# Kernel optimization log

Measured on AMD Instinct MI355X. Metric: run time of the kernel, lower is better.

## Reference

```python
import jax, jax.numpy as jnp
import numpy as np

B, N, C = 8, 1374, 768
H = 12
HD = C // H  # 64
HIDDEN = int(C * 4.0)  # 3072
EPS = 1e-5


def setup_inputs() -> dict:
    key = jax.random.key(0)
    ks = jax.random.split(key, 12)
    s = 0.02
    return {
        "x": jax.random.normal(ks[0], (B, N, C), jnp.float32),
        "rope_freqs": jax.random.normal(ks[1], (1, N, 1, HD), jnp.float32),
        "ln1_g": jnp.ones((C,), jnp.float32),
        "ln1_b": jnp.zeros((C,), jnp.float32),
        "qkv_w": jax.random.normal(ks[2], (3 * C, C), jnp.float32) * s,
        "qkv_b": jnp.zeros((3 * C,), jnp.float32),
        "proj_w": jax.random.normal(ks[3], (C, C), jnp.float32) * s,
        "proj_b": jnp.zeros((C,), jnp.float32),
        "ln2_g": jnp.ones((C,), jnp.float32),
        "ln2_b": jnp.zeros((C,), jnp.float32),
        "w1": jax.random.normal(ks[4], (HIDDEN, C), jnp.float32) * s,
        "b1": jnp.zeros((HIDDEN,), jnp.float32),
        "w2": jax.random.normal(ks[5], (HIDDEN, C), jnp.float32) * s,
        "b2": jnp.zeros((HIDDEN,), jnp.float32),
        "w3": jax.random.normal(ks[6], (C, HIDDEN), jnp.float32) * s,
        "b3": jnp.zeros((C,), jnp.float32),
    }


def _layernorm(x, g, b):
    mu = jnp.mean(x, axis=-1, keepdims=True)
    var = jnp.mean(jnp.square(x - mu), axis=-1, keepdims=True)
    return (x - mu) * jax.lax.rsqrt(var + EPS) * g + b


def _rotate_half(x):
    x1, x2 = jnp.split(x, 2, axis=-1)
    return jnp.concatenate([-x2, x1], axis=-1)


def _apply_rope(q, k, freqs):
    # freqs: [1, N, 1, HD] -> [1, 1, N, HD] (matches torch permute(0,2,1,3))
    f = jnp.transpose(freqs, (0, 2, 1, 3))
    cos, sin = jnp.cos(f), jnp.sin(f)
    q_rot = q * cos + _rotate_half(q) * sin
    k_rot = k * cos + _rotate_half(k) * sin
    return q_rot, k_rot


def reference(x, rope_freqs, ln1_g, ln1_b, qkv_w, qkv_b, proj_w, proj_b,
              ln2_g, ln2_b, w1, b1, w2, b2, w3, b3):
    scale = HD ** -0.5
    # --- Attention branch ---
    h = _layernorm(x, ln1_g, ln1_b)
    qkv = jnp.einsum('bnc,dc->bnd', h, qkv_w) + qkv_b          # [B,N,3C]
    qkv = qkv.reshape(B, N, 3, H, HD).transpose(2, 0, 3, 1, 4)  # [3,B,H,N,HD]
    q, k, v = qkv[0], qkv[1], qkv[2]
    # rope_freqs covers all N tokens -> n_special = 0 path
    q, k = _apply_rope(q, k, rope_freqs)
    attn = jnp.einsum('bhnd,bhmd->bhnm', q, k) * scale          # [B,H,N,N]
    attn = jax.nn.softmax(attn, axis=-1)
    o = jnp.einsum('bhnm,bhmd->bhnd', attn, v)                  # [B,H,N,HD]
    o = o.transpose(0, 2, 1, 3).reshape(B, N, C)
    o = jnp.einsum('bnc,dc->bnd', o, proj_w) + proj_b
    x = x + o
    # --- SwiGLU MLP branch ---
    h2 = _layernorm(x, ln2_g, ln2_b)
    x1 = jnp.einsum('bnc,hc->bnh', h2, w1) + b1
    x2 = jnp.einsum('bnc,hc->bnh', h2, w2) + b2
    hid = jax.nn.silu(x1) * x2
    mlp_out = jnp.einsum('bnh,ch->bnc', hid, w3) + b3
    return x + mlp_out
```

## Files before the change

### kernel.cpp

```cpp
#include <hip/hip_runtime.h>
#include <stdint.h>

#define B_ 8
#define N_ 1374
#define C_ 768
#define H_ 12
#define HD_ 64
#define HID_ 3072
#define M_ (B_*N_)
#define MPAD_ 11008
#define QT_ 22
#define QT2_ 11

#define QSC_ 0.18033688011112042f

typedef __attribute__((ext_vector_type(8))) short short8;
typedef __attribute__((ext_vector_type(4))) float f32x4;
typedef __attribute__((ext_vector_type(16))) float f32x16;
typedef __attribute__((ext_vector_type(4))) _Float16 half4;
typedef __attribute__((ext_vector_type(2))) _Float16 half2v;

__device__ __forceinline__ unsigned short f2bf(float f) {
  unsigned u = __float_as_uint(f);
  u += 0x7FFF + ((u >> 16) & 1);
  return (unsigned short)(u >> 16);
}
__device__ __forceinline__ float bf2f(unsigned short h) {
  return __uint_as_float(((unsigned)h) << 16);
}
__device__ __forceinline__ unsigned short f2h(float f) {
  return __builtin_bit_cast(unsigned short, (_Float16)f);
}

__device__ __forceinline__ half2v pkrtz(float a, float b) {
  return __builtin_bit_cast(half2v, __builtin_amdgcn_cvt_pkrtz(a, b));
}

#if __has_builtin(__builtin_amdgcn_global_load_lds)
#define HAVE_GLL 1
#endif

__device__ __forceinline__ void gld16(const unsigned short* g, unsigned short* l) {
#ifdef HAVE_GLL
  __builtin_amdgcn_global_load_lds((const __attribute__((address_space(1))) void*)g,
                                   (__attribute__((address_space(3))) void*)l, 16, 0, 0);
#else
  *(short8*)l = *(const short8*)g;
#endif
}

__device__ __forceinline__ void ln_body(const float* __restrict__ in,
    const float* __restrict__ g, const float* __restrict__ bta,
    unsigned short* __restrict__ out, int row, int t) {
  const float* xr = in + (size_t)row * C_;
  float v0 = xr[t], v1 = xr[t + 256], v2 = xr[t + 512];
  float s1 = v0 + v1 + v2;
  float s2 = v0*v0 + v1*v1 + v2*v2;
  for (int off = 1; off < 64; off <<= 1) {
    s1 += __shfl_xor(s1, off, 64);
    s2 += __shfl_xor(s2, off, 64);
  }
  __shared__ float r1[4], r2[4];
  int wave = t >> 6, lane = t & 63;
  if (lane == 0) { r1[wave] = s1; r2[wave] = s2; }
  __syncthreads();
  float tot1 = r1[0] + r1[1] + r1[2] + r1[3];
  float tot2 = r2[0] + r2[1] + r2[2] + r2[3];
  float mu = tot1 * (1.0f / C_);
  float var = tot2 * (1.0f / C_) - mu * mu;
  float rs = rsqrtf(var + 1e-5f);
  size_t ob = (size_t)row * C_;
  out[ob + t]       = f2bf((v0 - mu) * rs * g[t]       + bta[t]);
  out[ob + t + 256] = f2bf((v1 - mu) * rs * g[t + 256] + bta[t + 256]);
  out[ob + t + 512] = f2bf((v2 - mu) * rs * g[t + 512] + bta[t + 512]);
}

__global__ __launch_bounds__(256) void ln_kernel(const float* __restrict__ in,
    const float* __restrict__ g, const float* __restrict__ bta,
    unsigned short* __restrict__ out) {
  ln_body(in, g, bta, out, blockIdx.x, threadIdx.x);
}

__global__ __launch_bounds__(256) void cvt5_ln_kernel(
    const float* __restrict__ s0, const float* __restrict__ s1,
    const float* __restrict__ s2, const float* __restrict__ s3,
    const float* __restrict__ s4, unsigned short* __restrict__ out,
    const float* __restrict__ x, const float* __restrict__ ln_g,
    const float* __restrict__ ln_b, unsigned short* __restrict__ h) {
  int blk = blockIdx.x;
  if (blk < 9216) {
    int id = blk * 256 + threadIdx.x;
    const float* src; int off;
    if (id < 442368)        { src = s0; off = id; }
    else if (id < 589824)   { src = s1; off = id - 442368; }
    else if (id < 1179648)  { src = s2; off = id - 589824; }
    else if (id < 1769472)  { src = s3; off = id - 1179648; }
    else                    { src = s4; off = id - 1769472; }
    float4 v = ((const float4*)src)[off];
    ushort4 o;
    o.x = f2bf(v.x); o.y = f2bf(v.y); o.z = f2bf(v.z); o.w = f2bf(v.w);
    ((ushort4*)out)[id] = o;
  } else {
    ln_body(x, ln_g, ln_b, h, blk - 9216, threadIdx.x);
  }
}

template<int EPI, int ROPE, int TM, int SWZ>
__global__ __launch_bounds__(256, (TM == 64) ? 4 : 2) void gemm_bt(
    const unsigned short* __restrict__ A,
    const unsigned short* __restrict__ W,
    void* __restrict__ outp,
    const float* __restrict__ bias0,
    const float* __restrict__ resid,
    const float* __restrict__ freqs,
    int K, int ldo, int Mvalid, int X)
{
  constexpr int MI = TM / 32;
  __shared__ __align__(16) unsigned short As[2][TM * 32];
  __shared__ __align__(16) unsigned short Bs[2][4096];
  const int t = threadIdx.x;
  const int lane = t & 63;
  const int wave = t >> 6;
  const int wm = (wave >> 1) * (TM / 2);
  const int wn = (wave & 1) * 64;
  const int lr = lane & 15;
  const int lg = lane >> 4;
  const int lk = lg * 8;
  int bx, by;
  if (SWZ) {
    int Y = gridDim.x / X;
    int lin = blockIdx.x;
    int sgsz = X * 8;
    int sg = lin / sgsz;
    int base_y = sg * 8;
    int rows = Y - base_y; if (rows > 8) rows = 8;
    int within = lin - sg * sgsz;
    by = base_y + within % rows;
    bx = within / rows;
  } else {
    bx = blockIdx.x % X;
    by = blockIdx.x / X;
  }
  const int tm0 = by * TM;
  const int tn0 = bx * 128;
  const int r0 = t >> 2;
  const int c0 = (t & 3) * 8;
  const unsigned short* ga0 = A + (size_t)(tm0 + r0) * K + c0;
  const unsigned short* ga1 = A + (size_t)(tm0 + 64 + r0) * K + c0;
  const unsigned short* gb0 = W + (size_t)(tn0 + r0) * K + c0;
  const unsigned short* gb1 = W + (size_t)(tn0 + 64 + r0) * K + c0;
  f32x4 zero = {0.f, 0.f, 0.f, 0.f};
  f32x4 acc[MI][4];
#pragma unroll
  for (int mi = 0; mi < MI; ++mi)
#pragma unroll
    for (int ni = 0; ni < 4; ++ni) acc[mi][ni] = zero;

  for (int kt = 0; kt < K; kt += 64) {
    __syncthreads();
    gld16(ga0 + kt,      &As[0][t * 8]);
    gld16(ga0 + kt + 32, &As[1][t * 8]);
    if (TM == 128) {
      gld16(ga1 + kt,      &As[0][2048 + t * 8]);
      gld16(ga1 + kt + 32, &As[1][2048 + t * 8]);
    }
    gld16(gb0 + kt,      &Bs[0][t * 8]);
    gld16(gb1 + kt,      &Bs[0][2048 + t * 8]);
    gld16(gb0 + kt + 32, &Bs[1][t * 8]);
    gld16(gb1 + kt + 32, &Bs[1][2048 + t * 8]);
    __syncthreads();
#pragma unroll
    for (int u = 0; u < 2; ++u) {
      short8 af[MI], bfr[4];
#pragma unroll
      for (int mi = 0; mi < MI; ++mi) af[mi] = *(const short8*)&As[u][(wm + mi * 16 + lr) * 32 + lk];
#pragma unroll
      for (int ni = 0; ni < 4; ++ni) bfr[ni] = *(const short8*)&Bs[u][(wn + ni * 16 + lr) * 32 + lk];
#pragma unroll
      for (int mi = 0; mi < MI; ++mi)
#pragma unroll
        for (int ni = 0; ni < 4; ++ni)
          acc[mi][ni] = __builtin_amdgcn_mfma_f32_16x16x32_bf16(af[mi], bfr[ni], acc[mi][ni], 0, 0, 0);
    }
  }

  if (EPI == 0) {
    bool dorope = ROPE && ((tn0 + wn) < 1536);
    bool isq    = ROPE && ((tn0 + wn) < 768);
    bool isv    = ROPE && ((tn0 + wn) >= 1536);
#pragma unroll
    for (int mi = 0; mi < MI; ++mi) {
#pragma unroll
      for (int p = 0; p < 2; ++p) {
        int col1 = tn0 + wn + p * 16 + lr;
        int col2 = col1 + 32;
        float bv1 = bias0[col1], bv2 = bias0[col2];
        int e = p * 16 + lr;
#pragma unroll
        for (int r = 0; r < 4; ++r) {
          int row = tm0 + wm + mi * 16 + lg * 4 + r;
          float v1 = acc[mi][p][r] + bv1;
          float v2 = acc[mi][p + 2][r] + bv2;
          float o1 = v1, o2 = v2;
          if (dorope) {
            int n = row % N_;
            float f1 = freqs[n * HD_ + e];
            float f2 = freqs[n * HD_ + e + 32];
            float c1, s1, c2, s2;
            __sincosf(f1, &s1, &c1);
            __sincosf(f2, &s2, &c2);
            o1 = v1 * c1 - v2 * s1;
            o2 = v2 * c2 + v1 * s2;
          }
          if (isq) { o1 *= QSC_; o2 *= QSC_; }
          size_t base = (size_t)row * ldo;
          if (isv) {
            ((unsigned short*)outp)[base + col1] = f2h(o1);
            ((unsigned short*)outp)[base + col2] = f2h(o2);
          } else {
            ((unsigned short*)outp)[base + col1] = f2bf(o1);
            ((unsigned short*)outp)[base + col2] = f2bf(o2);
          }
        }
      }
    }
  } else {
#pragma unroll
    for (int mi = 0; mi < MI; ++mi) {
#pragma unroll
      for (int ni = 0; ni < 4; ++ni) {
        int col = tn0 + wn + ni * 16 + lr;
        float bval = bias0[col];
#pragma unroll
        for (int r = 0; r < 4; ++r) {
          int row = tm0 + wm + mi * 16 + lg * 4 + r;
          float v = acc[mi][ni][r] + bval;
          size_t idx = (size_t)row * ldo + col;
          if (EPI == 1) {
            if (row < Mvalid) ((float*)outp)[idx] = resid[idx] + v;
          } else {
            if (row < Mvalid) ((float*)outp)[idx] = ((float*)outp)[idx] + v;
          }
        }
      }
    }
  }
}

__global__ __launch_bounds__(256, 2) void gemm_w12_swiglu(
    const unsigned short* __restrict__ A,
    const unsigned short* __restrict__ W1,
    const unsigned short* __restrict__ W2,
    unsigned short* __restrict__ hid,
    const float* __restrict__ b1,
    const float* __restrict__ b2)
{
  __shared__ __align__(16) unsigned short As[2][4096];
  __shared__ __align__(16) unsigned short B1s[2][2048];
  __shared__ __align__(16) unsigned short B2s[2][2048];
  const int t = threadIdx.x;
  const int lane = t & 63;
  const int wave = t >> 6;
  const int wm = (wave >> 1) * 64;
  const int wn = (wave & 1) * 32;
  const int lr = lane & 15;
  const int lg = lane >> 4;
  const int lk = lg * 8;
  const int tm0 = blockIdx.y * 128;
  const int tn0 = blockIdx.x * 64;
  const int r0 = t >> 2;
  const int c0 = (t & 3) * 8;
  const unsigned short* ga0 = A + (size_t)(tm0 + r0) * 768 + c0;
  const unsigned short* ga1 = A + (size_t)(tm0 + 64 + r0) * 768 + c0;
  const unsigned short* g1 = W1 + (size_t)(tn0 + r0) * 768 + c0;
  const unsigned short* g2 = W2 + (size_t)(tn0 + r0) * 768 + c0;
  f32x4 zero = {0.f, 0.f, 0.f, 0.f};
  f32x4 acc1[4][2], acc2[4][2];
#pragma unroll
  for (int mi = 0; mi < 4; ++mi)
#pragma unroll
    for (int ni = 0; ni < 2; ++ni) { acc1[mi][ni] = zero; acc2[mi][ni] = zero; }

  for (int kt = 0; kt < 768; kt += 64) {
    __syncthreads();
    gld16(ga0 + kt,      &As[0][t * 8]);
    gld16(ga1 + kt,      &As[0][2048 + t * 8]);
    gld16(ga0 + kt + 32, &As[1][t * 8]);
    gld16(ga1 + kt + 32, &As[1][2048 + t * 8]);
    gld16(g1 + kt,       &B1s[0][t * 8]);
    gld16(g1 + kt + 32,  &B1s[1][t * 8]);
    gld16(g2 + kt,       &B2s[0][t * 8]);
    gld16(g2 + kt + 32,  &B2s[1][t * 8]);
    __syncthreads();
#pragma unroll
    for (int u = 0; u < 2; ++u) {
      short8 af[4], b1f[2], b2f[2];
#pragma unroll
      for (int mi = 0; mi < 4; ++mi) af[mi] = *(const short8*)&As[u][(wm + mi * 16 + lr) * 32 + lk];
#pragma unroll
      for (int ni = 0; ni < 2; ++ni) {
        b1f[ni] = *(const short8*)&B1s[u][(wn + ni * 16 + lr) * 32 + lk];
        b2f[ni] = *(const short8*)&B2s[u][(wn + ni * 16 + lr) * 32 + lk];
      }
#pragma unroll
      for (int mi = 0; mi < 4; ++mi)
#pragma unroll
        for (int ni = 0; ni < 2; ++ni) {
          acc1[mi][ni] = __builtin_amdgcn_mfma_f32_16x16x32_bf16(af[mi], b1f[ni], acc1[mi][ni], 0, 0, 0);
          acc2[mi][ni] = __builtin_amdgcn_mfma_f32_16x16x32_bf16(af[mi], b2f[ni], acc2[mi][ni], 0, 0, 0);
        }
    }
  }
#pragma unroll
  for (int mi = 0; mi < 4; ++mi) {
#pragma unroll
    for (int ni = 0; ni < 2; ++ni) {
      int col = tn0 + wn + ni * 16 + lr;
      float bv1 = b1[col], bv2 = b2[col];
#pragma unroll
      for (int r = 0; r < 4; ++r) {
        int row = tm0 + wm + mi * 16 + lg * 4 + r;
        float a1 = acc1[mi][ni][r] + bv1;
        float a2 = acc2[mi][ni][r] + bv2;
        float h = a1 / (1.f + __expf(-a1)) * a2;
        hid[(size_t)row * HID_ + col] = f2bf(h);
      }
    }
  }
}

struct FalseT { static constexpr bool value = false; };
struct TrueT  { static constexpr bool value = true;  };

__global__ __launch_bounds__(256, 3) void attn_kernel(
    const unsigned short* __restrict__ qkv,
    unsigned short* __restrict__ o2)
{
  __shared__ __align__(16) unsigned short Ks[2][64 * 88];
  __shared__ __align__(16) _Float16 Vt[2][64 * 72];
  int bidx = blockIdx.x;
  int qt = bidx % QT2_;
  int bh = bidx / QT2_;
  int head = bh % H_;
  int b = bh / H_;
  int t = threadIdx.x, lane = t & 63, wave = t >> 6;
  int lq = lane & 31, lg2 = lane >> 5;

  short8 bq[4];
  {
    int m = qt * 128 + wave * 32 + lq;
    int mc = (m < N_) ? m : (N_ - 1);
    const unsigned short* qrow = qkv + (size_t)(b * N_ + mc) * 2304 + head * HD_;
#pragma unroll
    for (int c = 0; c < 4; ++c)
      bq[c] = *(const short8*)(qrow + c * 16 + lg2 * 8);
  }

  f32x16 acc[2];
  f32x16 dacc;
  acc[0] = {}; acc[1] = {}; dacc = {};

  const int kr0 = t >> 3;
  const int kc  = (t & 7) * 8;
  const int vp  = t & 31;
  const int vc  = t >> 5;
  const unsigned short* kbase = qkv + (size_t)(b * N_) * 2304 + 768  + head * HD_ + kc;
  const unsigned short* vbase = qkv + (size_t)(b * N_) * 2304 + 1536 + head * HD_ + vc * 8;

  short8 krg[2], vrg[2];
  auto issue = [&](int jt) {
    int j0 = jt * 64 + kr0;        if (j0 >= N_) j0 = N_ - 1;
    int j1 = jt * 64 + kr0 + 32;   if (j1 >= N_) j1 = N_ - 1;
    int vj0 = jt * 64 + 2 * vp;    if (vj0 >= N_) vj0 = N_ - 1;
    int vj1 = jt * 64 + 2 * vp + 1; if (vj1 >= N_) vj1 = N_ - 1;
    krg[0] = *(const short8*)(kbase + (size_t)j0 * 2304);
    krg[1] = *(const short8*)(kbase + (size_t)j1 * 2304);
    vrg[0] = *(const short8*)(vbase + (size_t)vj0 * 2304);
    vrg[1] = *(const short8*)(vbase + (size_t)vj1 * 2304);
  };

  const half4 vones = {(_Float16)1.f, (_Float16)1.f, (_Float16)1.f, (_Float16)1.f};

  auto compute = [&](int jt, const unsigned short* ksb, const _Float16* vtb, auto tailc) {
    constexpr bool TAIL = decltype(tailc)::value;
#pragma unroll
    for (int st2 = 0; st2 < 2; ++st2) {
      f32x16 sc = {};
      {
        const unsigned short* krow = &ksb[(st2 * 32 + lq) * 88 + lg2 * 8];
        short8 ak0 = *(const short8*)(krow);
        short8 ak1 = *(const short8*)(krow + 16);
        short8 ak2 = *(const short8*)(krow + 32);
        short8 ak3 = *(const short8*)(krow + 48);
        sc = __builtin_amdgcn_mfma_f32_32x32x16_bf16(ak0, bq[0], sc, 0, 0, 0);
        sc = __builtin_amdgcn_mfma_f32_32x32x16_bf16(ak1, bq[1], sc, 0, 0, 0);
        sc = __builtin_amdgcn_mfma_f32_32x32x16_bf16(ak2, bq[2], sc, 0, 0, 0);
        sc = __builtin_amdgcn_mfma_f32_32x32x16_bf16(ak3, bq[3], sc, 0, 0, 0);
      }
#pragma unroll
      for (int r = 0; r < 16; ++r) {
        float pv = exp2f(sc[r]);
        if (TAIL) {
          int jw = (r & 3) + 8 * (r >> 2) + 4 * lg2;
          int j = jt * 64 + st2 * 32 + jw;
          pv = (j < N_) ? pv : 0.f;
        }
        sc[r] = pv;
      }
      half4 pf[4];
#pragma unroll
      for (int ks = 0; ks < 4; ++ks) {
        union { half4 v; half2v h[2]; } pu;
        pu.h[0] = pkrtz(sc[ks * 4 + 0], sc[ks * 4 + 1]);
        pu.h[1] = pkrtz(sc[ks * 4 + 2], sc[ks * 4 + 3]);
        pf[ks] = pu.v;
      }
#pragma unroll
      for (int ks = 0; ks < 4; ++ks)
        dacc = __builtin_amdgcn_mfma_f32_32x32x8f16(pf[ks], vones, dacc, 0, 0, 0);
#pragma unroll
      for (int dt = 0; dt < 2; ++dt) {
#pragma unroll
        for (int ks = 0; ks < 4; ++ks) {
          half4 bv = *(const half4*)&vtb[(dt * 32 + lq) * 72 + st2 * 32 + ks * 8 + lg2 * 4];
          acc[dt] = __builtin_amdgcn_mfma_f32_32x32x8f16(pf[ks], bv, acc[dt], 0, 0, 0);
        }
      }
    }
  };

  issue(0);
  int cur = 0;
  for (int jt = 0; jt < QT_; ++jt) {
    unsigned short* ksb = &Ks[cur][0];
    _Float16* vtb = &Vt[cur][0];
    *(short8*)&ksb[kr0 * 88 + kc] = krg[0];
    *(short8*)&ksb[(kr0 + 32) * 88 + kc] = krg[1];
#pragma unroll
    for (int i = 0; i < 8; ++i) {
      unsigned lo = (unsigned short)vrg[0][i];
      unsigned hi = (unsigned short)vrg[1][i];
      *(unsigned*)&Vt[cur][(vc * 8 + i) * 72 + 2 * vp] = lo | (hi << 16);
    }
    __syncthreads();
    issue(jt + 1);
    if (jt == QT_ - 1) compute(jt, ksb, vtb, TrueT{});
    else               compute(jt, ksb, vtb, FalseT{});
    cur ^= 1;
  }

#pragma unroll
  for (int r = 0; r < 16; ++r) {
    int qw = (r & 3) + 8 * (r >> 2) + 4 * lg2;
    int m = qt * 128 + wave * 32 + qw;
    if (m < N_) {
      float invd = 1.f / dacc[r];
      unsigned short* orow = o2 + (size_t)(b * N_ + m) * C_ + head * HD_ + lq;
      orow[0]  = f2bf(acc[0][r] * invd);
      orow[32] = f2bf(acc[1][r] * invd);
    }
  }
}

extern "C" void kernel_launch(void* const* d_in, const int* in_sizes, int n_in,
                              void* d_out, int out_size, void* d_ws, size_t ws_size,
                              hipStream_t stream) {
  const float* x      = (const float*)d_in[0];
  const float* freqs  = (const float*)d_in[1];
  const float* ln1_g  = (const float*)d_in[2];
  const float* ln1_b  = (const float*)d_in[3];
  const float* qkv_w  = (const float*)d_in[4];
  const float* qkv_b  = (const float*)d_in[5];
  const float* proj_w = (const float*)d_in[6];
  const float* proj_b = (const float*)d_in[7];
  const float* ln2_g  = (const float*)d_in[8];
  const float* ln2_b  = (const float*)d_in[9];
  const float* w1     = (const float*)d_in[10];
  const float* b1     = (const float*)d_in[11];
  const float* w2     = (const float*)d_in[12];
  const float* b2     = (const float*)d_in[13];
  const float* w3     = (const float*)d_in[14];
  const float* b3     = (const float*)d_in[15];
  float* out = (float*)d_out;
  char* ws = (char*)d_ws;

  unsigned short* hB     = (unsigned short*)(ws + 0);
  unsigned short* wqkvB  = (unsigned short*)(ws + 16908288);
  unsigned short* wprojB = (unsigned short*)(ws + 20447232);
  unsigned short* w12B   = (unsigned short*)(ws + 21626880);
  unsigned short* w3B    = (unsigned short*)(ws + 31064064);
  unsigned short* qkvB   = (unsigned short*)(ws + 35782656);
  unsigned short* o2B    = (unsigned short*)(ws + 86507520);
  unsigned short* hidB   = qkvB;

  cvt5_ln_kernel<<<9216 + M_, 256, 0, stream>>>(qkv_w, proj_w, w1, w2, w3, wqkvB,
                                                x, ln1_g, ln1_b, hB);

  gemm_bt<0, 1, 128, 1><<<18 * 86, 256, 0, stream>>>(hB, wqkvB, qkvB, qkv_b, nullptr, freqs, 768, 2304, M_, 18);
  attn_kernel<<<B_ * H_ * QT2_, 256, 0, stream>>>(qkvB, o2B);
  gemm_bt<1, 0, 64, 1><<<6 * 172, 256, 0, stream>>>(o2B, wprojB, out, proj_b, x, nullptr, 768, 768, M_, 6);

  ln_kernel<<<M_, 256, 0, stream>>>(out, ln2_g, ln2_b, hB);
  gemm_w12_swiglu<<<dim3(48, 86), 256, 0, stream>>>(hB, w12B, w12B + 3072 * 768, hidB, b1, b2);
  gemm_bt<3, 0, 128, 1><<<6 * 86, 256, 0, stream>>>(hidB, w3B, out, b3, nullptr, nullptr, 3072, 768, M_, 6);
}
```

Measured before the change: 526.7 us.

## Interleave W1/W2 rows and use 256x256 eight-wave pipelined SwiGLU GEMM

Weight conversion now interleaves W1 and W2 in 128-row blocks, so one 256-column tile of the combined weight covers matching halves of both projections. The SwiGLU GEMM is replaced by a 512-thread kernel with 256x256 tiles, a double-buffered 128KB LDS pipeline, explicit vmcnt waits, barriers and setprio around the MFMA blocks. The W2 half of the accumulators is exchanged through LDS for the epilogue. The aim is higher arithmetic intensity and latency hiding, at the cost of one block per CU from LDS use, fewer blocks overall, and fragile hand-scheduled synchronisation.

```diff
diff --git a/kernel.cpp b/kernel.cpp
--- a/kernel.cpp
+++ b/kernel.cpp
@@ -90,16 +90,26 @@
   int blk = blockIdx.x;
   if (blk < 9216) {
     int id = blk * 256 + threadIdx.x;
-    const float* src; int off;
+    const float* src; int off; int dest = id;
     if (id < 442368)        { src = s0; off = id; }
     else if (id < 589824)   { src = s1; off = id - 442368; }
-    else if (id < 1179648)  { src = s2; off = id - 589824; }
-    else if (id < 1769472)  { src = s3; off = id - 1179648; }
+    else if (id < 1179648)  {
+      src = s2; off = id - 589824;
+      int r = off / 192, c = off % 192;
+      int rho = ((r >> 7) << 8) + (r & 127);
+      dest = 589824 + rho * 192 + c;
+    }
+    else if (id < 1769472)  {
+      src = s3; off = id - 1179648;
+      int r = off / 192, c = off % 192;
+      int rho = ((r >> 7) << 8) + 128 + (r & 127);
+      dest = 589824 + rho * 192 + c;
+    }
     else                    { src = s4; off = id - 1769472; }
     float4 v = ((const float4*)src)[off];
     ushort4 o;
     o.x = f2bf(v.x); o.y = f2bf(v.y); o.z = f2bf(v.z); o.w = f2bf(v.w);
-    ((ushort4*)out)[id] = o;
+    ((ushort4*)out)[dest] = o;
   } else {
     ln_body(x, ln_g, ln_b, h, blk - 9216, threadIdx.x);
   }
@@ -247,83 +257,127 @@
   }
 }
 
-__global__ __launch_bounds__(256, 2) void gemm_w12_swiglu(
+__global__ __launch_bounds__(512, 2) void gemm_w12_8p(
     const unsigned short* __restrict__ A,
-    const unsigned short* __restrict__ W1,
-    const unsigned short* __restrict__ W2,
+    const unsigned short* __restrict__ Wi,
     unsigned short* __restrict__ hid,
     const float* __restrict__ b1,
     const float* __restrict__ b2)
 {
-  __shared__ __align__(16) unsigned short As[2][4096];
-  __shared__ __align__(16) unsigned short B1s[2][2048];
-  __shared__ __align__(16) unsigned short B2s[2][2048];
+  __shared__ __align__(16) unsigned short SH[65536];
   const int t = threadIdx.x;
   const int lane = t & 63;
   const int wave = t >> 6;
-  const int wm = (wave >> 1) * 64;
-  const int wn = (wave & 1) * 32;
+  const int wm = (wave >> 2) * 128;
+  const int wn = (wave & 3) * 64;
   const int lr = lane & 15;
   const int lg = lane >> 4;
-  const int lk = lg * 8;
-  const int tm0 = blockIdx.y * 128;
-  const int tn0 = blockIdx.x * 64;
-  const int r0 = t >> 2;
-  const int c0 = (t & 3) * 8;
-  const unsigned short* ga0 = A + (size_t)(tm0 + r0) * 768 + c0;
-  const unsigned short* ga1 = A + (size_t)(tm0 + 64 + r0) * 768 + c0;
-  const unsigned short* g1 = W1 + (size_t)(tn0 + r0) * 768 + c0;
-  const unsigned short* g2 = W2 + (size_t)(tn0 + r0) * 768 + c0;
-  f32x4 zero = {0.f, 0.f, 0.f, 0.f};
-  f32x4 acc1[4][2], acc2[4][2];
-#pragma unroll
-  for (int mi = 0; mi < 4; ++mi)
-#pragma unroll
-    for (int ni = 0; ni < 2; ++ni) { acc1[mi][ni] = zero; acc2[mi][ni] = zero; }
-
-  for (int kt = 0; kt < 768; kt += 64) {
-    __syncthreads();
-    gld16(ga0 + kt,      &As[0][t * 8]);
-    gld16(ga1 + kt,      &As[0][2048 + t * 8]);
-    gld16(ga0 + kt + 32, &As[1][t * 8]);
-    gld16(ga1 + kt + 32, &As[1][2048 + t * 8]);
-    gld16(g1 + kt,       &B1s[0][t * 8]);
-    gld16(g1 + kt + 32,  &B1s[1][t * 8]);
-    gld16(g2 + kt,       &B2s[0][t * 8]);
-    gld16(g2 + kt + 32,  &B2s[1][t * 8]);
-    __syncthreads();
-#pragma unroll
-    for (int u = 0; u < 2; ++u) {
-      short8 af[4], b1f[2], b2f[2];
-#pragma unroll
-      for (int mi = 0; mi < 4; ++mi) af[mi] = *(const short8*)&As[u][(wm + mi * 16 + lr) * 32 + lk];
-#pragma unroll
-      for (int ni = 0; ni < 2; ++ni) {
-        b1f[ni] = *(const short8*)&B1s[u][(wn + ni * 16 + lr) * 32 + lk];
-        b2f[ni] = *(const short8*)&B2s[u][(wn + ni * 16 + lr) * 32 + lk];
-      }
-#pragma unroll
-      for (int mi = 0; mi < 4; ++mi)
-#pragma unroll
-        for (int ni = 0; ni < 2; ++ni) {
-          acc1[mi][ni] = __builtin_amdgcn_mfma_f32_16x16x32_bf16(af[mi], b1f[ni], acc1[mi][ni], 0, 0, 0);
-          acc2[mi][ni] = __builtin_amdgcn_mfma_f32_16x16x32_bf16(af[mi], b2f[ni], acc2[mi][ni], 0, 0, 0);
+  const int bx = blockIdx.x % 24;
+  const int by = blockIdx.x / 24;
+  const int tm0 = by * 256;
+  const int tn0 = bx * 256;
+
+  auto plane = [&](int buf, int op, int ks) -> unsigned short* {
+    return SH + buf * 32768 + op * 16384 + ks * 8192;
+  };
+  auto stageHT = [&](int tile, int op, int ks) {
+    if (tile >= 12) return;
+    const unsigned short* src = op ? Wi : A;
+    int rb = op ? tn0 : tm0;
+    unsigned short* pl = plane(tile & 1, op, ks);
+    int kc = tile * 64 + ks * 32;
+#pragma unroll
+    for (int g = 0; g < 2; ++g) {
+      int s = g * 512 + t;
+      int row = s >> 2;
+      int c16 = s & 3;
+      gld16(src + (size_t)(rb + row) * 768 + kc + c16 * 8, pl + s * 8);
+    }
+  };
+
+  f32x4 acc[8][4];
+#pragma unroll
+  for (int mi = 0; mi < 8; ++mi)
+#pragma unroll
+    for (int ni = 0; ni < 4; ++ni) acc[mi][ni] = f32x4{0.f, 0.f, 0.f, 0.f};
+
+  stageHT(0, 0, 0); stageHT(0, 1, 0); stageHT(0, 0, 1); stageHT(0, 1, 1);
+  stageHT(1, 0, 0); stageHT(1, 1, 0);
+  asm volatile("s_waitcnt vmcnt(4)" ::: "memory");
+  __builtin_amdgcn_s_barrier();
+
+  for (int it = 0; it < 6; ++it) {
+    int T = it * 2;
+#pragma unroll
+    for (int ph = 0; ph < 8; ++ph) {
+      const int tile = (ph < 4) ? T : T + 1;
+      const int buf = tile & 1;
+      const int ks = (ph >> 1) & 1;
+      const int mh = ph & 1;
+      short8 af[4], bfr[4];
+      const unsigned short* Ap = plane(buf, 0, ks);
+      const unsigned short* Bp = plane(buf, 1, ks);
+#pragma unroll
+      for (int i = 0; i < 4; ++i) {
+        af[i]  = *(const short8*)&Ap[(wm + (mh * 4 + i) * 16 + lr) * 32 + lg * 8];
+        bfr[i] = *(const short8*)&Bp[(wn + i * 16 + lr) * 32 + lg * 8];
+      }
+      switch (ph) {
+        case 0: stageHT(T + 1, 0, 1); break;
+        case 1: stageHT(T + 1, 1, 1); break;
+        case 2: stageHT(T + 2, 0, 0); break;
+        case 3: stageHT(T + 2, 1, 0); break;
+        case 4: stageHT(T + 2, 0, 1); break;
+        case 5: stageHT(T + 2, 1, 1); break;
+        case 6: stageHT(T + 3, 0, 0); break;
+        case 7: stageHT(T + 3, 1, 0); break;
+      }
+      __builtin_amdgcn_s_barrier();
+      asm volatile("s_waitcnt lgkmcnt(0)" ::: "memory");
+      __builtin_amdgcn_sched_barrier(0);
+      __builtin_amdgcn_s_setprio(1);
+#pragma unroll
+      for (int i = 0; i < 4; ++i)
+#pragma unroll
+        for (int ni = 0; ni < 4; ++ni)
+          acc[mh * 4 + i][ni] = __builtin_amdgcn_mfma_f32_16x16x32_bf16(
+              af[i], bfr[ni], acc[mh * 4 + i][ni], 0, 0, 0);
+      __builtin_amdgcn_s_setprio(0);
+      if (ph == 3 || ph == 7)
+        asm volatile("s_waitcnt vmcnt(4)" ::: "memory");
+      __builtin_amdgcn_s_barrier();
+    }
+  }
+
+  __syncthreads();
+  float* X2 = (float*)SH;
+  if ((wave & 3) >= 2) {
+    int cb = wn - 128;
+#pragma unroll
+    for (int mi = 0; mi < 8; ++mi)
+#pragma unroll
+      for (int ni = 0; ni < 4; ++ni)
+#pragma unroll
+        for (int r = 0; r < 4; ++r)
+          X2[(wm + mi * 16 + lg * 4 + r) * 128 + cb + ni * 16 + lr] = acc[mi][ni][r];
+  }
+  __syncthreads();
+  if ((wave & 3) < 2) {
+#pragma unroll
+    for (int mi = 0; mi < 8; ++mi) {
+#pragma unroll
+      for (int ni = 0; ni < 4; ++ni) {
+        int cl = wn + ni * 16 + lr;
+        float bv1 = b1[bx * 128 + cl];
+        float bv2 = b2[bx * 128 + cl];
+#pragma unroll
+        for (int r = 0; r < 4; ++r) {
+          int rl = wm + mi * 16 + lg * 4 + r;
+          float a1 = acc[mi][ni][r] + bv1;
+          float a2 = X2[rl * 128 + cl] + bv2;
+          float h = a1 / (1.f + __expf(-a1)) * a2;
+          hid[(size_t)(tm0 + rl) * HID_ + bx * 128 + cl] = f2bf(h);
         }
-    }
-  }
-#pragma unroll
-  for (int mi = 0; mi < 4; ++mi) {
-#pragma unroll
-    for (int ni = 0; ni < 2; ++ni) {
-      int col = tn0 + wn + ni * 16 + lr;
-      float bv1 = b1[col], bv2 = b2[col];
-#pragma unroll
-      for (int r = 0; r < 4; ++r) {
-        int row = tm0 + wm + mi * 16 + lg * 4 + r;
-        float a1 = acc1[mi][ni][r] + bv1;
-        float a2 = acc2[mi][ni][r] + bv2;
-        float h = a1 / (1.f + __expf(-a1)) * a2;
-        hid[(size_t)row * HID_ + col] = f2bf(h);
       }
     }
   }
@@ -501,6 +555,6 @@
   gemm_bt<1, 0, 64, 1><<<6 * 172, 256, 0, stream>>>(o2B, wprojB, out, proj_b, x, nullptr, 768, 768, M_, 6);
 
   ln_kernel<<<M_, 256, 0, stream>>>(out, ln2_g, ln2_b, hB);
-  gemm_w12_swiglu<<<dim3(48, 86), 256, 0, stream>>>(hB, w12B, w12B + 3072 * 768, hidB, b1, b2);
+  gemm_w12_8p<<<43 * 24, 512, 0, stream>>>(hB, w12B, hidB, b1, b2);
   gemm_bt<3, 0, 128, 1><<<6 * 86, 256, 0, stream>>>(hidB, w3B, out, b3, nullptr, nullptr, 3072, 768, M_, 6);
 }
```

Measured after the change: 603.4 us. 14.6% more time.
